# Kernel optimization log

Hardware: AMD Instinct MI355X
Metric: run time of the kernel (lower is better)

Reference implementation:

```python
import jax, jax.numpy as jnp
import numpy as np

B, T, H = 1024, 256, 128

def _gru(x, Wx, Wh, b):
    # Keras GRU (reset_after=True), gate order z, r, h. x: [B,T,D], b: [2,3H]
    xp = x @ Wx + b[0]                      # [B,T,3H]
    h0 = jnp.zeros((x.shape[0], Wh.shape[0]), x.dtype)
    def step(h, xt):
        hp = h @ Wh + b[1]
        xz, xr, xh = jnp.split(xt, 3, axis=-1)
        hz, hr, hn = jnp.split(hp, 3, axis=-1)
        z = jax.nn.sigmoid(xz + hz)
        r = jax.nn.sigmoid(xr + hr)
        hh = jnp.tanh(xh + r * hn)
        return z * h + (1.0 - z) * hh, None
    h, _ = jax.lax.scan(step, h0, jnp.swapaxes(xp, 0, 1))
    return h                                 # [B,H]

def setup_inputs() -> dict:
    key = jax.random.key(0)
    ks = jax.random.split(key, 32)
    def gp(k, shape, scale=0.05):
        return (jax.random.normal(k, shape, dtype=jnp.float32) * scale)
    inp = {
        "spatial": jax.random.normal(ks[0], (B, T, 2), dtype=jnp.float32),
        "hour_idx": jax.random.randint(ks[1], (B, T), 0, 24, dtype=jnp.int32),
        "week_idx": jax.random.randint(ks[2], (B, T), 0, 7, dtype=jnp.int32),
        "E_time": gp(ks[3], (24, H)),
        "E_week": gp(ks[4], (7, H)),
        # spatial GRU (input dim 2)
        "Ws_x": gp(ks[5], (2, 3 * H)), "Ws_h": gp(ks[6], (H, 3 * H)), "bs": gp(ks[7], (2, 3 * H)),
        # hour temporal GRU (input dim 128)
        "Wh_x": gp(ks[8], (H, 3 * H)), "Wh_h": gp(ks[9], (H, 3 * H)), "bh": gp(ks[10], (2, 3 * H)),
        # week temporal GRU (input dim 128)
        "Ww_x": gp(ks[11], (H, 3 * H)), "Ww_h": gp(ks[12], (H, 3 * H)), "bw": gp(ks[13], (2, 3 * H)),
        # attention Dense(3) over the channel axis of size 3
        "Wa": gp(ks[14], (3, 3)), "ba": gp(ks[15], (3,)),
        # MLP
        "W1": gp(ks[16], (H, 1024)), "b1": gp(ks[17], (1024,)),
        "W2": gp(ks[18], (1024, 512)), "b2": gp(ks[19], (512,)),
        "W3": gp(ks[20], (512, 256)), "b3": gp(ks[21], (256,)),
        "W4": gp(ks[22], (256, H)), "b4": gp(ks[23], (H,)),
        "Wo": gp(ks[24], (H, 1)), "bo": gp(ks[25], (1,)),
    }
    return inp

def reference(spatial, hour_idx, week_idx, E_time, E_week,
              Ws_x, Ws_h, bs, Wh_x, Wh_h, bh, Ww_x, Ww_h, bw,
              Wa, ba, W1, b1, W2, b2, W3, b3, W4, b4, Wo, bo):
    te = E_time[hour_idx]                    # [B,T,128] gather
    we = E_week[week_idx]                    # [B,T,128] gather
    fs = _gru(spatial, Ws_x, Ws_h, bs)       # [B,128]
    fh = _gru(te, Wh_x, Wh_h, bh)            # [B,128]
    fw = _gru(we, Ww_x, Ww_h, bw)            # [B,128]
    allf = jnp.stack([fs, fh, fw], axis=-1)  # [B,128,3]
    scores = jax.nn.softmax(jax.nn.relu(allf @ Wa + ba), axis=-1)
    sf = jnp.sum(allf * scores, axis=-1)     # [B,128] attention-fused features
    x = jax.nn.relu(sf @ W1 + b1)
    x = jax.nn.relu(x @ W2 + b2)
    x = jax.nn.relu(x @ W3 + b3)
    x = jax.nn.relu(x @ W4 + b4)
    out = (x + sf) @ Wo + bo                 # residual then Dense(1)
    return out[:, 0]                         # [B]
```

## Files before the change

kernel.cpp:

```cpp
#include <hip/hip_runtime.h>
#include <hip/hip_bf16.h>

typedef __attribute__((ext_vector_type(8))) short short8;
typedef __attribute__((ext_vector_type(4))) float f32x4;
typedef __attribute__((ext_vector_type(2))) float f32x2;

#define LOG2E  1.44269504088896340736f
#define NLOG2E (-1.44269504088896340736f)
#define TLOG2E (2.88539008177792681472f)

#define HES 168

__device__ __forceinline__ unsigned short f2bf(float f) {
  unsigned u = __builtin_bit_cast(unsigned, f);
  u += 0x7fffu + ((u >> 16) & 1u);
  return (unsigned short)(u >> 16);
}

__global__ __launch_bounds__(256) void setup_kernel(
    const float* __restrict__ E_time, const float* __restrict__ E_week,
    const float* __restrict__ Wh_x, const float* __restrict__ bh,
    const float* __restrict__ Ww_x, const float* __restrict__ bw,
    const float* __restrict__ W1, const float* __restrict__ W2,
    const float* __restrict__ W3, const float* __restrict__ W4,
    float* __restrict__ Ptime, float* __restrict__ Pweek,
    unsigned short* __restrict__ Wt)
{
  const int b = blockIdx.x;
  const int tid = threadIdx.x;
  if (b < 31) {
    for (int c = tid; c < 384; c += 256) {
      if (b < 24) {
        float acc = bh[c];
        for (int d = 0; d < 128; ++d)
          acc = fmaf(E_time[b * 128 + d], Wh_x[d * 384 + c], acc);
        Ptime[b * 384 + c] = acc;
      } else {
        const int r = b - 24;
        float acc = bw[c];
        for (int d = 0; d < 128; ++d)
          acc = fmaf(E_week[r * 128 + d], Ww_x[d * 384 + c], acc);
        Pweek[r * 384 + c] = acc;
      }
    }
    return;
  }
  __shared__ float tile[64][65];
  int tb = b - 31;
  const float* src; unsigned short* dst; int K, N, tk, tn;
  if (tb < 32)       { src = W1; dst = Wt;          K = 128;  N = 1024; tk = tb >> 4; tn = tb & 15; }
  else if (tb < 160) { tb -= 32;  src = W2; dst = Wt + 131072; K = 1024; N = 512;  tk = tb >> 3; tn = tb & 7; }
  else if (tb < 192) { tb -= 160; src = W3; dst = Wt + 655360; K = 512;  N = 256;  tk = tb >> 2; tn = tb & 3; }
  else               { tb -= 192; src = W4; dst = Wt + 786432; K = 256;  N = 128;  tk = tb >> 1; tn = tb & 1; }
  const int tx = tid & 63, ty = tid >> 6;
  const int k0 = tk * 64, n0 = tn * 64;
  #pragma unroll
  for (int i = 0; i < 16; ++i)
    tile[ty * 16 + i][tx] = src[(k0 + ty * 16 + i) * N + n0 + tx];
  __syncthreads();
  #pragma unroll
  for (int i = 0; i < 16; ++i)
    dst[(n0 + ty * 16 + i) * K + k0 + tx] = f2bf(tile[tx][ty * 16 + i]);
}

__global__ __launch_bounds__(512, 2) void gru_kernel(
    const float* __restrict__ spatial,
    const int* __restrict__ hour_idx,
    const int* __restrict__ week_idx,
    const float* __restrict__ Ws_x,
    const float* __restrict__ Ws_h, const float* __restrict__ bs,
    const float* __restrict__ Wh_h, const float* __restrict__ bh,
    const float* __restrict__ Ww_h, const float* __restrict__ bw,
    const float* __restrict__ Ptime, const float* __restrict__ Pweek,
    float* __restrict__ fs, float* __restrict__ fh, float* __restrict__ fw)
{
  __shared__ __align__(16) unsigned short hx[2][16 * HES];

  const int tid  = threadIdx.x;
  const int lane = tid & 63;
  const int wv   = tid >> 6;
  const int ar   = lane & 15;
  const int akg  = lane >> 4;
  const int gid  = blockIdx.x;
  const int gru  = gid >> 6;
  const int row0 = (gid & 63) * 16;

  const float* __restrict__ Wh   = (gru == 0) ? Ws_h : (gru == 1) ? Wh_h : Ww_h;
  const float* __restrict__ bvec = (gru == 0) ? bs   : (gru == 1) ? bh   : bw;
  float* __restrict__ fout       = (gru == 0) ? fs   : (gru == 1) ? fh   : fw;
  const float* __restrict__ Ptab = (gru == 1) ? Ptime : Pweek;
  const int* __restrict__ idxg   = (gru == 1) ? hour_idx : week_idx;
  const int NR = (gru == 1) ? 24 : 7;

  const int j = wv * 16 + ar;

  short8 wf[15];
  #pragma unroll
  for (int g = 0; g < 2; ++g) {
    #pragma unroll
    for (int ks = 0; ks < 5; ++ks) {
      short8 f;
      #pragma unroll
      for (int q = 0; q < 8; ++q) {
        const int k = ks * 32 + akg * 8 + q;
        float v;
        if (k < 128) v = Wh[k * 384 + g * 128 + j];
        else {
          const int p = k - 128;
          if (gru == 0) v = (p == 0) ? Ws_x[g * 128 + j]
                          : (p == 1) ? Ws_x[384 + g * 128 + j] : 0.f;
          else          v = (p < NR) ? Ptab[p * 384 + g * 128 + j] : 0.f;
        }
        f[q] = (short)f2bf(v * NLOG2E);
      }
      wf[g * 5 + ks] = f;
    }
  }
  #pragma unroll
  for (int ks = 0; ks < 4; ++ks) {
    short8 f;
    #pragma unroll
    for (int q = 0; q < 8; ++q) {
      const int k = ks * 32 + akg * 8 + q;
      f[q] = (short)f2bf(Wh[k * 384 + 256 + j] * TLOG2E);
    }
    wf[10 + ks] = f;
  }
  {
    short8 f;
    #pragma unroll
    for (int q = 0; q < 8; ++q) {
      const int p = akg * 8 + q;
      float v;
      if (gru == 0) v = (p == 0) ? Ws_x[256 + j]
                      : (p == 1) ? Ws_x[384 + 256 + j] : 0.f;
      else          v = (p < NR) ? Ptab[p * 384 + 256 + j] : 0.f;
      f[q] = (short)f2bf(v * TLOG2E);
    }
    wf[14] = f;
  }

  const float bz  = (bvec[384 + j]       + (gru == 0 ? bvec[j]       : 0.f)) * NLOG2E;
  const float br  = (bvec[384 + 128 + j] + (gru == 0 ? bvec[128 + j] : 0.f)) * NLOG2E;
  const float bnh = bvec[384 + 256 + j] * TLOG2E;
  const float bnx = (gru == 0 ? bvec[256 + j] : 0.f) * TLOG2E;

  for (int e = tid; e < 2 * 16 * HES; e += 512) ((unsigned short*)hx)[e] = 0;
  __syncthreads();

  const bool mt  = (tid & 31) == 0;
  const int mrow = tid >> 5;
  int ix_prev = 0, ix_cur = 0;
  if (mt) {
    if (gru == 0) {
      const f32x2 s = *(const f32x2*)&spatial[(row0 + mrow) * 512];
      unsigned pk;
      asm("v_cvt_pk_bf16_f32 %0, %1, %2" : "=v"(pk) : "v"(s.x), "v"(s.y));
      *(unsigned*)&hx[0][mrow * HES + 128] = pk;
    } else {
      ix_cur = idxg[(row0 + mrow) * 256];
      hx[0][mrow * HES + 128 + ix_cur] = 0x3F80;
    }
  }
  __syncthreads();

  float hst[4] = {0.f, 0.f, 0.f, 0.f};

  for (int t = 0; t < 256; ++t) {
    const unsigned short* __restrict__ hb = hx[t & 1];
    unsigned short* __restrict__ ho       = hx[(t + 1) & 1];

    short8 a[5];
    #pragma unroll
    for (int ks = 0; ks < 5; ++ks)
      a[ks] = *(const short8*)&hb[ar * HES + ks * 32 + akg * 8];

    f32x2 msp = {0.f, 0.f};
    int ix_next = 0;
    const bool mact = mt && (t + 1 < 256);
    if (mact) {
      if (gru == 0) msp = *(const f32x2*)&spatial[(row0 + mrow) * 512 + 2 * (t + 1)];
      else          ix_next = idxg[(row0 + mrow) * 256 + t + 1];
    }

    f32x4 az  = {bz, bz, bz, bz};
    f32x4 arr = {br, br, br, br};
    f32x4 anh = {bnh, bnh, bnh, bnh};
    f32x4 anx = {bnx, bnx, bnx, bnx};
    #pragma unroll
    for (int ks = 0; ks < 4; ++ks) {
      az  = __builtin_amdgcn_mfma_f32_16x16x32_bf16(a[ks], wf[ks],      az,  0, 0, 0);
      arr = __builtin_amdgcn_mfma_f32_16x16x32_bf16(a[ks], wf[5 + ks],  arr, 0, 0, 0);
      anh = __builtin_amdgcn_mfma_f32_16x16x32_bf16(a[ks], wf[10 + ks], anh, 0, 0, 0);
    }
    az  = __builtin_amdgcn_mfma_f32_16x16x32_bf16(a[4], wf[4],  az,  0, 0, 0);
    arr = __builtin_amdgcn_mfma_f32_16x16x32_bf16(a[4], wf[9],  arr, 0, 0, 0);
    anx = __builtin_amdgcn_mfma_f32_16x16x32_bf16(a[4], wf[14], anx, 0, 0, 0);

    if (mact) {
      if (gru == 0) {
        unsigned pk;
        asm("v_cvt_pk_bf16_f32 %0, %1, %2" : "=v"(pk) : "v"(msp.x), "v"(msp.y));
        *(unsigned*)&ho[mrow * HES + 128] = pk;
      } else {
        if (t >= 1) ho[mrow * HES + 128 + ix_prev] = 0;
        ho[mrow * HES + 128 + ix_next] = 0x3F80;
        ix_prev = ix_cur; ix_cur = ix_next;
      }
    }

    float pz[4], pr[4];
    #pragma unroll
    for (int q = 0; q < 4; ++q) {
      pz[q] = 1.f + __builtin_amdgcn_exp2f(az[q]);
      pr[q] = 1.f + __builtin_amdgcn_exp2f(arr[q]);
    }
    float zg[4], rg[4];
    #pragma unroll
    for (int p = 0; p < 4; p += 2) {
      const float A0 = pz[p] * pr[p];
      const float A1 = pz[p + 1] * pr[p + 1];
      const float inv = __builtin_amdgcn_rcpf(A0 * A1);
      const float t1 = A1 * inv, t0 = A0 * inv;
      zg[p]     = pr[p] * t1;     rg[p]     = pz[p] * t1;
      zg[p + 1] = pr[p + 1] * t0; rg[p + 1] = pz[p + 1] * t0;
    }
    float ph[4];
    #pragma unroll
    for (int q = 0; q < 4; ++q)
      ph[q] = 1.f + __builtin_amdgcn_exp2f(fmaf(rg[q], anh[q], anx[q]));
    float hn4[4];
    #pragma unroll
    for (int p = 0; p < 4; p += 2) {
      const float inv = __builtin_amdgcn_rcpf(ph[p] * ph[p + 1]);
      const float hh0 = fmaf(-2.f, ph[p + 1] * inv, 1.f);
      const float hh1 = fmaf(-2.f, ph[p] * inv, 1.f);
      hn4[p]     = fmaf(zg[p],     hst[p]     - hh0, hh0);
      hn4[p + 1] = fmaf(zg[p + 1], hst[p + 1] - hh1, hh1);
      hst[p] = hn4[p]; hst[p + 1] = hn4[p + 1];
    }

    #pragma unroll
    for (int q = 0; q < 4; ++q)
      ho[(akg * 4 + q) * HES + j] = f2bf(hn4[q]);

    __syncthreads();
  }

  #pragma unroll
  for (int q = 0; q < 4; ++q)
    fout[(row0 + akg * 4 + q) * 128 + j] = hst[q];
}

template<int K, int N>
__device__ __forceinline__ void mlp_layer(
    const unsigned short* __restrict__ xin, unsigned short* __restrict__ xout,
    const unsigned short* __restrict__ Wt, const float* __restrict__ bias,
    int lane, int wv, float* __restrict__ foutF)
{
  constexpr int NT = N / 64;
  const int ar  = lane & 15;
  const int akg = lane >> 4;
  f32x4 acc[NT];
  #pragma unroll
  for (int nt = 0; nt < NT; ++nt) acc[nt] = f32x4{0.f, 0.f, 0.f, 0.f};
  for (int ks = 0; ks < K / 32; ++ks) {
    const short8 a = *(const short8*)&xin[ar * 1032 + ks * 32 + akg * 8];
    #pragma unroll
    for (int nt = 0; nt < NT; ++nt) {
      const int n = wv * (N / 4) + nt * 16 + ar;
      const short8 b = *(const short8*)&Wt[n * K + ks * 32 + akg * 8];
      acc[nt] = __builtin_amdgcn_mfma_f32_16x16x32_bf16(a, b, acc[nt], 0, 0, 0);
    }
  }
  const int rbase = akg * 4;
  #pragma unroll
  for (int nt = 0; nt < NT; ++nt) {
    const int n = wv * (N / 4) + nt * 16 + ar;
    const float bv = bias[n];
    #pragma unroll
    for (int q = 0; q < 4; ++q) {
      float v = acc[nt][q] + bv;
      v = fmaxf(v, 0.f);
      xout[(rbase + q) * 1032 + n] = f2bf(v);
      if (foutF) foutF[(rbase + q) * 128 + n] = v;
    }
  }
}

__global__ __launch_bounds__(256) void attn_mlp_kernel(
    const float* __restrict__ fs, const float* __restrict__ fh, const float* __restrict__ fw,
    const float* __restrict__ Wa, const float* __restrict__ ba,
    const unsigned short* __restrict__ Wt,
    const float* __restrict__ b1, const float* __restrict__ b2,
    const float* __restrict__ b3, const float* __restrict__ b4,
    const float* __restrict__ Wo, const float* __restrict__ bo,
    float* __restrict__ out)
{
  __shared__ __align__(16) unsigned short xa[16 * 1032];
  __shared__ __align__(16) unsigned short xb[16 * 1032];
  __shared__ __align__(16) float sf_l[16 * 128];
  __shared__ __align__(16) float x4f[16 * 128];

  const int tid  = threadIdx.x;
  const int lane = tid & 63;
  const int wv   = tid >> 6;
  const int row0 = blockIdx.x * 16;

  {
    const int i  = tid >> 4;
    const int j0 = (tid & 15) * 8;
    float wa[9], bav[3];
    #pragma unroll
    for (int q = 0; q < 9; ++q) wa[q] = Wa[q];
    #pragma unroll
    for (int q = 0; q < 3; ++q) bav[q] = ba[q];
    const int base = (row0 + i) * 128 + j0;
    #pragma unroll
    for (int half = 0; half < 2; ++half) {
      const f32x4 a = *(const f32x4*)&fs[base + half * 4];
      const f32x4 b = *(const f32x4*)&fh[base + half * 4];
      const f32x4 c = *(const f32x4*)&fw[base + half * 4];
      #pragma unroll
      for (int q = 0; q < 4; ++q) {
        const float f0 = a[q], f1 = b[q], f2 = c[q];
        float s0 = f0 * wa[0] + f1 * wa[3] + f2 * wa[6] + bav[0];
        float s1 = f0 * wa[1] + f1 * wa[4] + f2 * wa[7] + bav[1];
        float s2 = f0 * wa[2] + f1 * wa[5] + f2 * wa[8] + bav[2];
        s0 = fmaxf(s0, 0.f); s1 = fmaxf(s1, 0.f); s2 = fmaxf(s2, 0.f);
        const float m  = fmaxf(s0, fmaxf(s1, s2));
        const float e0 = __builtin_amdgcn_exp2f((s0 - m) * LOG2E);
        const float e1 = __builtin_amdgcn_exp2f((s1 - m) * LOG2E);
        const float e2 = __builtin_amdgcn_exp2f((s2 - m) * LOG2E);
        const float inv = __builtin_amdgcn_rcpf(e0 + e1 + e2);
        const float sf  = (f0 * e0 + f1 * e1 + f2 * e2) * inv;
        const int jj = j0 + half * 4 + q;
        sf_l[i * 128 + jj] = sf;
        xa[i * 1032 + jj]  = f2bf(sf);
      }
    }
  }
  __syncthreads();

  mlp_layer<128, 1024>(xa, xb, Wt,          b1, lane, wv, nullptr);
  __syncthreads();
  mlp_layer<1024, 512>(xb, xa, Wt + 131072, b2, lane, wv, nullptr);
  __syncthreads();
  mlp_layer<512,  256>(xa, xb, Wt + 655360, b3, lane, wv, nullptr);
  __syncthreads();
  mlp_layer<256,  128>(xb, xa, Wt + 786432, b4, lane, wv, x4f);
  __syncthreads();

  const int row = tid >> 4;
  const int p   = tid & 15;
  float part = 0.f;
  #pragma unroll
  for (int q = 0; q < 8; ++q) {
    const int jj = p + q * 16;
    part += (x4f[row * 128 + jj] + sf_l[row * 128 + jj]) * Wo[jj];
  }
  #pragma unroll
  for (int off = 8; off > 0; off >>= 1)
    part += __shfl_xor(part, off, 16);
  if (p == 0) out[row0 + row] = part + bo[0];
}

extern "C" void kernel_launch(void* const* d_in, const int* in_sizes, int n_in,
                              void* d_out, int out_size, void* d_ws, size_t ws_size,
                              hipStream_t stream) {
  const float* spatial  = (const float*)d_in[0];
  const int*   hour_idx = (const int*)d_in[1];
  const int*   week_idx = (const int*)d_in[2];
  const float* E_time   = (const float*)d_in[3];
  const float* E_week   = (const float*)d_in[4];
  const float* Ws_x = (const float*)d_in[5];
  const float* Ws_h = (const float*)d_in[6];
  const float* bs   = (const float*)d_in[7];
  const float* Wh_x = (const float*)d_in[8];
  const float* Wh_h = (const float*)d_in[9];
  const float* bh   = (const float*)d_in[10];
  const float* Ww_x = (const float*)d_in[11];
  const float* Ww_h = (const float*)d_in[12];
  const float* bw   = (const float*)d_in[13];
  const float* Wa   = (const float*)d_in[14];
  const float* ba   = (const float*)d_in[15];
  const float* W1   = (const float*)d_in[16];
  const float* b1   = (const float*)d_in[17];
  const float* W2   = (const float*)d_in[18];
  const float* b2   = (const float*)d_in[19];
  const float* W3   = (const float*)d_in[20];
  const float* b3   = (const float*)d_in[21];
  const float* W4   = (const float*)d_in[22];
  const float* b4   = (const float*)d_in[23];
  const float* Wo   = (const float*)d_in[24];
  const float* bo   = (const float*)d_in[25];
  float* out = (float*)d_out;

  float* ws    = (float*)d_ws;
  float* Ptime = ws;
  float* Pweek = Ptime + 9216;
  float* fsb   = Pweek + 2688;
  float* fhb   = fsb + 131072;
  float* fwb   = fhb + 131072;
  unsigned short* Wt = (unsigned short*)(fwb + 131072);

  setup_kernel<<<231, 256, 0, stream>>>(E_time, E_week, Wh_x, bh, Ww_x, bw,
      W1, W2, W3, W4, Ptime, Pweek, Wt);
  gru_kernel<<<192, 512, 0, stream>>>(spatial, hour_idx, week_idx, Ws_x,
      Ws_h, bs, Wh_h, bh, Ww_h, bw, Ptime, Pweek, fsb, fhb, fwb);
  attn_mlp_kernel<<<64, 256, 0, stream>>>(fsb, fhb, fwb, Wa, ba, Wt,
      b1, b2, b3, b4, Wo, bo, out);
}
```

Before: 240.1 us.

## Move MLP weight transpose into GRU kernel tail and widen MLP blocks

```diff
diff --git a/kernel.cpp b/kernel.cpp
--- a/kernel.cpp
+++ b/kernel.cpp
@@ -4,6 +4,7 @@
 typedef __attribute__((ext_vector_type(8))) short short8;
 typedef __attribute__((ext_vector_type(4))) float f32x4;
 typedef __attribute__((ext_vector_type(2))) float f32x2;
+typedef __attribute__((ext_vector_type(2))) unsigned u32x2;
 
 #define LOG2E  1.44269504088896340736f
 #define NLOG2E (-1.44269504088896340736f)
@@ -17,50 +18,27 @@
   return (unsigned short)(u >> 16);
 }
 
-__global__ __launch_bounds__(256) void setup_kernel(
+__global__ __launch_bounds__(256) void ptab_kernel(
     const float* __restrict__ E_time, const float* __restrict__ E_week,
     const float* __restrict__ Wh_x, const float* __restrict__ bh,
     const float* __restrict__ Ww_x, const float* __restrict__ bw,
-    const float* __restrict__ W1, const float* __restrict__ W2,
-    const float* __restrict__ W3, const float* __restrict__ W4,
-    float* __restrict__ Ptime, float* __restrict__ Pweek,
-    unsigned short* __restrict__ Wt)
+    float* __restrict__ Ptime, float* __restrict__ Pweek)
 {
   const int b = blockIdx.x;
-  const int tid = threadIdx.x;
-  if (b < 31) {
-    for (int c = tid; c < 384; c += 256) {
-      if (b < 24) {
-        float acc = bh[c];
-        for (int d = 0; d < 128; ++d)
-          acc = fmaf(E_time[b * 128 + d], Wh_x[d * 384 + c], acc);
-        Ptime[b * 384 + c] = acc;
-      } else {
-        const int r = b - 24;
-        float acc = bw[c];
-        for (int d = 0; d < 128; ++d)
-          acc = fmaf(E_week[r * 128 + d], Ww_x[d * 384 + c], acc);
-        Pweek[r * 384 + c] = acc;
-      }
-    }
-    return;
-  }
-  __shared__ float tile[64][65];
-  int tb = b - 31;
-  const float* src; unsigned short* dst; int K, N, tk, tn;
-  if (tb < 32)       { src = W1; dst = Wt;          K = 128;  N = 1024; tk = tb >> 4; tn = tb & 15; }
-  else if (tb < 160) { tb -= 32;  src = W2; dst = Wt + 131072; K = 1024; N = 512;  tk = tb >> 3; tn = tb & 7; }
-  else if (tb < 192) { tb -= 160; src = W3; dst = Wt + 655360; K = 512;  N = 256;  tk = tb >> 2; tn = tb & 3; }
-  else               { tb -= 192; src = W4; dst = Wt + 786432; K = 256;  N = 128;  tk = tb >> 1; tn = tb & 1; }
-  const int tx = tid & 63, ty = tid >> 6;
-  const int k0 = tk * 64, n0 = tn * 64;
-  #pragma unroll
-  for (int i = 0; i < 16; ++i)
-    tile[ty * 16 + i][tx] = src[(k0 + ty * 16 + i) * N + n0 + tx];
-  __syncthreads();
-  #pragma unroll
-  for (int i = 0; i < 16; ++i)
-    dst[(n0 + ty * 16 + i) * K + k0 + tx] = f2bf(tile[tx][ty * 16 + i]);
+  for (int c = threadIdx.x; c < 384; c += 256) {
+    if (b < 24) {
+      float acc = bh[c];
+      for (int d = 0; d < 128; ++d)
+        acc = fmaf(E_time[b * 128 + d], Wh_x[d * 384 + c], acc);
+      Ptime[b * 384 + c] = acc;
+    } else {
+      const int r = b - 24;
+      float acc = bw[c];
+      for (int d = 0; d < 128; ++d)
+        acc = fmaf(E_week[r * 128 + d], Ww_x[d * 384 + c], acc);
+      Pweek[r * 384 + c] = acc;
+    }
+  }
 }
 
 __global__ __launch_bounds__(512, 2) void gru_kernel(
@@ -72,9 +50,13 @@
     const float* __restrict__ Wh_h, const float* __restrict__ bh,
     const float* __restrict__ Ww_h, const float* __restrict__ bw,
     const float* __restrict__ Ptime, const float* __restrict__ Pweek,
+    const float* __restrict__ W1, const float* __restrict__ W2,
+    const float* __restrict__ W3, const float* __restrict__ W4,
+    unsigned short* __restrict__ Wt,
     float* __restrict__ fs, float* __restrict__ fh, float* __restrict__ fw)
 {
-  __shared__ __align__(16) unsigned short hx[2][16 * HES];
+  __shared__ __align__(16) unsigned char smem_u[64 * 65 * 4];
+  unsigned short (*hx)[16 * HES] = (unsigned short (*)[16 * HES])smem_u;
 
   const int tid  = threadIdx.x;
   const int lane = tid & 63;
@@ -92,7 +74,8 @@
   const int* __restrict__ idxg   = (gru == 1) ? hour_idx : week_idx;
   const int NR = (gru == 1) ? 24 : 7;
 
-  const int j = wv * 16 + ar;
+  const int j  = wv * 16 + ar;
+  const int c4 = wv * 16 + akg * 4;
 
   short8 wf[15];
   #pragma unroll
@@ -140,10 +123,22 @@
     wf[14] = f;
   }
 
-  const float bz  = (bvec[384 + j]       + (gru == 0 ? bvec[j]       : 0.f)) * NLOG2E;
-  const float br  = (bvec[384 + 128 + j] + (gru == 0 ? bvec[128 + j] : 0.f)) * NLOG2E;
-  const float bnh = bvec[384 + 256 + j] * TLOG2E;
-  const float bnx = (gru == 0 ? bvec[256 + j] : 0.f) * TLOG2E;
+  f32x4 bzv, brv, bnhv, bnxv;
+  {
+    const f32x4 z1 = *(const f32x4*)&bvec[384 + c4];
+    const f32x4 r1 = *(const f32x4*)&bvec[384 + 128 + c4];
+    const f32x4 n1 = *(const f32x4*)&bvec[384 + 256 + c4];
+    if (gru == 0) {
+      const f32x4 z0 = *(const f32x4*)&bvec[c4];
+      const f32x4 r0 = *(const f32x4*)&bvec[128 + c4];
+      const f32x4 n0 = *(const f32x4*)&bvec[256 + c4];
+      bzv = (z1 + z0) * NLOG2E; brv = (r1 + r0) * NLOG2E;
+      bnhv = n1 * TLOG2E;       bnxv = n0 * TLOG2E;
+    } else {
+      bzv = z1 * NLOG2E; brv = r1 * NLOG2E;
+      bnhv = n1 * TLOG2E; bnxv = f32x4{0.f, 0.f, 0.f, 0.f};
+    }
+  }
 
   for (int e = tid; e < 2 * 16 * HES; e += 512) ((unsigned short*)hx)[e] = 0;
   __syncthreads();
@@ -170,10 +165,10 @@
     const unsigned short* __restrict__ hb = hx[t & 1];
     unsigned short* __restrict__ ho       = hx[(t + 1) & 1];
 
-    short8 a[5];
+    short8 b[5];
     #pragma unroll
     for (int ks = 0; ks < 5; ++ks)
-      a[ks] = *(const short8*)&hb[ar * HES + ks * 32 + akg * 8];
+      b[ks] = *(const short8*)&hb[ar * HES + ks * 32 + akg * 8];
 
     f32x2 msp = {0.f, 0.f};
     int ix_next = 0;
@@ -183,19 +178,19 @@
       else          ix_next = idxg[(row0 + mrow) * 256 + t + 1];
     }
 
-    f32x4 az  = {bz, bz, bz, bz};
-    f32x4 arr = {br, br, br, br};
-    f32x4 anh = {bnh, bnh, bnh, bnh};
-    f32x4 anx = {bnx, bnx, bnx, bnx};
+    f32x4 az  = bzv;
+    f32x4 arr = brv;
+    f32x4 anh = bnhv;
+    f32x4 anx = bnxv;
     #pragma unroll
     for (int ks = 0; ks < 4; ++ks) {
-      az  = __builtin_amdgcn_mfma_f32_16x16x32_bf16(a[ks], wf[ks],      az,  0, 0, 0);
-      arr = __builtin_amdgcn_mfma_f32_16x16x32_bf16(a[ks], wf[5 + ks],  arr, 0, 0, 0);
-      anh = __builtin_amdgcn_mfma_f32_16x16x32_bf16(a[ks], wf[10 + ks], anh, 0, 0, 0);
-    }
-    az  = __builtin_amdgcn_mfma_f32_16x16x32_bf16(a[4], wf[4],  az,  0, 0, 0);
-    arr = __builtin_amdgcn_mfma_f32_16x16x32_bf16(a[4], wf[9],  arr, 0, 0, 0);
-    anx = __builtin_amdgcn_mfma_f32_16x16x32_bf16(a[4], wf[14], anx, 0, 0, 0);
+      az  = __builtin_amdgcn_mfma_f32_16x16x32_bf16(wf[ks],      b[ks], az,  0, 0, 0);
+      arr = __builtin_amdgcn_mfma_f32_16x16x32_bf16(wf[5 + ks],  b[ks], arr, 0, 0, 0);
+      anh = __builtin_amdgcn_mfma_f32_16x16x32_bf16(wf[10 + ks], b[ks], anh, 0, 0, 0);
+    }
+    az  = __builtin_amdgcn_mfma_f32_16x16x32_bf16(wf[4],  b[4], az,  0, 0, 0);
+    arr = __builtin_amdgcn_mfma_f32_16x16x32_bf16(wf[9],  b[4], arr, 0, 0, 0);
+    anx = __builtin_amdgcn_mfma_f32_16x16x32_bf16(wf[14], b[4], anx, 0, 0, 0);
 
     if (mact) {
       if (gru == 0) {
@@ -240,16 +235,39 @@
       hst[p] = hn4[p]; hst[p + 1] = hn4[p + 1];
     }
 
-    #pragma unroll
-    for (int q = 0; q < 4; ++q)
-      ho[(akg * 4 + q) * HES + j] = f2bf(hn4[q]);
+    unsigned p01, p23;
+    asm("v_cvt_pk_bf16_f32 %0, %1, %2" : "=v"(p01) : "v"(hn4[0]), "v"(hn4[1]));
+    asm("v_cvt_pk_bf16_f32 %0, %1, %2" : "=v"(p23) : "v"(hn4[2]), "v"(hn4[3]));
+    *(u32x2*)&ho[ar * HES + c4] = u32x2{p01, p23};
 
     __syncthreads();
   }
 
-  #pragma unroll
-  for (int q = 0; q < 4; ++q)
-    fout[(row0 + akg * 4 + q) * 128 + j] = hst[q];
+  {
+    const f32x4 v = {hst[0], hst[1], hst[2], hst[3]};
+    *(f32x4*)&fout[(row0 + ar) * 128 + c4] = v;
+  }
+
+  __syncthreads();
+  float (*ttile)[65] = (float (*)[65])smem_u;
+  const int tx = tid & 63, ty = tid >> 6;
+  for (int t0 = blockIdx.x; t0 < 200; t0 += 192) {
+    int tb = t0;
+    const float* src; unsigned short* dst; int K, N, tk, tn;
+    if (tb < 32)       { src = W1; dst = Wt;          K = 128;  N = 1024; tk = tb >> 4; tn = tb & 15; }
+    else if (tb < 160) { tb -= 32;  src = W2; dst = Wt + 131072; K = 1024; N = 512;  tk = tb >> 3; tn = tb & 7; }
+    else if (tb < 192) { tb -= 160; src = W3; dst = Wt + 655360; K = 512;  N = 256;  tk = tb >> 2; tn = tb & 3; }
+    else               { tb -= 192; src = W4; dst = Wt + 786432; K = 256;  N = 128;  tk = tb >> 1; tn = tb & 1; }
+    const int k0 = tk * 64, n0 = tn * 64;
+    #pragma unroll
+    for (int i = 0; i < 8; ++i)
+      ttile[ty * 8 + i][tx] = src[(k0 + ty * 8 + i) * N + n0 + tx];
+    __syncthreads();
+    #pragma unroll
+    for (int i = 0; i < 8; ++i)
+      dst[(n0 + ty * 8 + i) * K + k0 + tx] = f2bf(ttile[tx][ty * 8 + i]);
+    __syncthreads();
+  }
 }
 
 template<int K, int N>
@@ -258,7 +276,7 @@
     const unsigned short* __restrict__ Wt, const float* __restrict__ bias,
     int lane, int wv, float* __restrict__ foutF)
 {
-  constexpr int NT = N / 64;
+  constexpr int NT = N / 128;
   const int ar  = lane & 15;
   const int akg = lane >> 4;
   f32x4 acc[NT];
@@ -268,7 +286,7 @@
     const short8 a = *(const short8*)&xin[ar * 1032 + ks * 32 + akg * 8];
     #pragma unroll
     for (int nt = 0; nt < NT; ++nt) {
-      const int n = wv * (N / 4) + nt * 16 + ar;
+      const int n = wv * (N / 8) + nt * 16 + ar;
       const short8 b = *(const short8*)&Wt[n * K + ks * 32 + akg * 8];
       acc[nt] = __builtin_amdgcn_mfma_f32_16x16x32_bf16(a, b, acc[nt], 0, 0, 0);
     }
@@ -276,7 +294,7 @@
   const int rbase = akg * 4;
   #pragma unroll
   for (int nt = 0; nt < NT; ++nt) {
-    const int n = wv * (N / 4) + nt * 16 + ar;
+    const int n = wv * (N / 8) + nt * 16 + ar;
     const float bv = bias[n];
     #pragma unroll
     for (int q = 0; q < 4; ++q) {
@@ -288,7 +306,7 @@
   }
 }
 
-__global__ __launch_bounds__(256) void attn_mlp_kernel(
+__global__ __launch_bounds__(512) void attn_mlp_kernel(
     const float* __restrict__ fs, const float* __restrict__ fh, const float* __restrict__ fw,
     const float* __restrict__ Wa, const float* __restrict__ ba,
     const unsigned short* __restrict__ Wt,
@@ -308,36 +326,33 @@
   const int row0 = blockIdx.x * 16;
 
   {
-    const int i  = tid >> 4;
-    const int j0 = (tid & 15) * 8;
+    const int i  = tid >> 5;
+    const int j0 = (tid & 31) * 4;
     float wa[9], bav[3];
     #pragma unroll
     for (int q = 0; q < 9; ++q) wa[q] = Wa[q];
     #pragma unroll
     for (int q = 0; q < 3; ++q) bav[q] = ba[q];
     const int base = (row0 + i) * 128 + j0;
-    #pragma unroll
-    for (int half = 0; half < 2; ++half) {
-      const f32x4 a = *(const f32x4*)&fs[base + half * 4];
-      const f32x4 b = *(const f32x4*)&fh[base + half * 4];
-      const f32x4 c = *(const f32x4*)&fw[base + half * 4];
-      #pragma unroll
-      for (int q = 0; q < 4; ++q) {
-        const float f0 = a[q], f1 = b[q], f2 = c[q];
-        float s0 = f0 * wa[0] + f1 * wa[3] + f2 * wa[6] + bav[0];
-        float s1 = f0 * wa[1] + f1 * wa[4] + f2 * wa[7] + bav[1];
-        float s2 = f0 * wa[2] + f1 * wa[5] + f2 * wa[8] + bav[2];
-        s0 = fmaxf(s0, 0.f); s1 = fmaxf(s1, 0.f); s2 = fmaxf(s2, 0.f);
-        const float m  = fmaxf(s0, fmaxf(s1, s2));
-        const float e0 = __builtin_amdgcn_exp2f((s0 - m) * LOG2E);
-        const float e1 = __builtin_amdgcn_exp2f((s1 - m) * LOG2E);
-        const float e2 = __builtin_amdgcn_exp2f((s2 - m) * LOG2E);
-        const float inv = __builtin_amdgcn_rcpf(e0 + e1 + e2);
-        const float sf  = (f0 * e0 + f1 * e1 + f2 * e2) * inv;
-        const int jj = j0 + half * 4 + q;
-        sf_l[i * 128 + jj] = sf;
-        xa[i * 1032 + jj]  = f2bf(sf);
-      }
+    const f32x4 a = *(const f32x4*)&fs[base];
+    const f32x4 b = *(const f32x4*)&fh[base];
+    const f32x4 c = *(const f32x4*)&fw[base];
+    #pragma unroll
+    for (int q = 0; q < 4; ++q) {
+      const float f0 = a[q], f1 = b[q], f2 = c[q];
+      float s0 = f0 * wa[0] + f1 * wa[3] + f2 * wa[6] + bav[0];
+      float s1 = f0 * wa[1] + f1 * wa[4] + f2 * wa[7] + bav[1];
+      float s2 = f0 * wa[2] + f1 * wa[5] + f2 * wa[8] + bav[2];
+      s0 = fmaxf(s0, 0.f); s1 = fmaxf(s1, 0.f); s2 = fmaxf(s2, 0.f);
+      const float m  = fmaxf(s0, fmaxf(s1, s2));
+      const float e0 = __builtin_amdgcn_exp2f((s0 - m) * LOG2E);
+      const float e1 = __builtin_amdgcn_exp2f((s1 - m) * LOG2E);
+      const float e2 = __builtin_amdgcn_exp2f((s2 - m) * LOG2E);
+      const float inv = __builtin_amdgcn_rcpf(e0 + e1 + e2);
+      const float sf  = (f0 * e0 + f1 * e1 + f2 * e2) * inv;
+      const int jj = j0 + q;
+      sf_l[i * 128 + jj] = sf;
+      xa[i * 1032 + jj]  = f2bf(sf);
     }
   }
   __syncthreads();
@@ -351,17 +366,17 @@
   mlp_layer<256,  128>(xb, xa, Wt + 786432, b4, lane, wv, x4f);
   __syncthreads();
 
-  const int row = tid >> 4;
-  const int p   = tid & 15;
+  const int row = tid >> 5;
+  const int p   = tid & 31;
   float part = 0.f;
   #pragma unroll
-  for (int q = 0; q < 8; ++q) {
-    const int jj = p + q * 16;
+  for (int q = 0; q < 4; ++q) {
+    const int jj = p + q * 32;
     part += (x4f[row * 128 + jj] + sf_l[row * 128 + jj]) * Wo[jj];
   }
   #pragma unroll
-  for (int off = 8; off > 0; off >>= 1)
-    part += __shfl_xor(part, off, 16);
+  for (int off = 16; off > 0; off >>= 1)
+    part += __shfl_xor(part, off, 32);
   if (p == 0) out[row0 + row] = part + bo[0];
 }
 
@@ -404,10 +419,10 @@
   float* fwb   = fhb + 131072;
   unsigned short* Wt = (unsigned short*)(fwb + 131072);
 
-  setup_kernel<<<231, 256, 0, stream>>>(E_time, E_week, Wh_x, bh, Ww_x, bw,
-      W1, W2, W3, W4, Ptime, Pweek, Wt);
+  ptab_kernel<<<31, 256, 0, stream>>>(E_time, E_week, Wh_x, bh, Ww_x, bw, Ptime, Pweek);
   gru_kernel<<<192, 512, 0, stream>>>(spatial, hour_idx, week_idx, Ws_x,
-      Ws_h, bs, Wh_h, bh, Ww_h, bw, Ptime, Pweek, fsb, fhb, fwb);
-  attn_mlp_kernel<<<64, 256, 0, stream>>>(fsb, fhb, fwb, Wa, ba, Wt,
+      Ws_h, bs, Wh_h, bh, Ww_h, bw, Ptime, Pweek,
+      W1, W2, W3, W4, Wt, fsb, fhb, fwb);
+  attn_mlp_kernel<<<64, 512, 0, stream>>>(fsb, fhb, fwb, Wa, ba, Wt,
       b1, b2, b3, b4, Wo, bo, out);
 }
```

Measured after the change: 230.5 us. -4.0%, faster.
